# Kernel tuning notes

Hardware: AMD Instinct MI355X
Metric: run time of the kernel (lower is better)

## Reference

```python
import jax, jax.numpy as jnp
import numpy as np

K = 256
ALPHA = 0.2   # bml_alpha
BETA = 0.3    # bml_beta
EPS = 1e-8    # torch CosineSimilarity eps
NEG_INF = -10000.0
WEIGHT_TEMP = 0.05


def _l2n(x):
    # cosine-normalize rows, matching nn.CosineSimilarity's eps clamp
    n = jnp.linalg.norm(x, axis=-1, keepdims=True)
    return x / jnp.maximum(n, EPS)


def setup_inputs() -> dict:
    key = jax.random.key(0)
    k1, k2, k3 = jax.random.split(key, 3)
    B, D = 8192, 768
    datapoints = jax.random.normal(k1, (B, D), dtype=jnp.float32)
    centroid = jax.random.normal(k2, (K, D), dtype=jnp.float32)
    batch_cos_sim = jax.random.normal(k3, (B, B), dtype=jnp.float32)
    return {"datapoints": datapoints, "centroid": centroid, "batch_cos_sim": batch_cos_sim}


def reference(datapoints, centroid, batch_cos_sim):
    B = datapoints.shape[0]
    datapoints = jax.lax.stop_gradient(datapoints)  # forward() does clone().detach()

    # intra_cos_sim = cos(datapoints, centroid) / temp (temp=1)  -> [B, K]
    intra_cos_sim = _l2n(datapoints) @ _l2n(centroid).T

    # cluster assignment + intra-class adjacency
    dp_index = jnp.argmax(intra_cos_sim, axis=-1)                 # [B]
    onehot = jax.nn.one_hot(dp_index, K, dtype=jnp.float32)       # [B, K]
    dp_cluster = onehot @ onehot.T                                # [B, B]
    eye = jnp.eye(B, dtype=bool)
    dp_cluster = jnp.where(eye, 0.0, dp_cluster)                  # fill_diagonal_(0)

    # gather assigned centroid per datapoint
    dp_centroid = centroid[dp_index]                              # [B, D]

    # hard negative: 2nd-closest centroid (top-2 on cosine sim), detached
    _, top2_idx = jax.lax.top_k(intra_cos_sim, 2)                 # [B, 2]
    hard_negative = jax.lax.stop_gradient(centroid[top2_idx[:, 1]])  # [B, D]

    # false-negative BML loss on the in-batch cosine matrix
    pos = jnp.diagonal(batch_cos_sim)[:, None]                    # [B, 1]
    delta = (batch_cos_sim - pos) * dp_cluster                    # [B, B]
    fn_loss = (jax.nn.relu(delta + ALPHA) + jax.nn.relu(-delta - BETA)).mean()

    # softmax-weighted negatives (diag masked to -10000), detached
    masked = jnp.where(eye, NEG_INF, batch_cos_sim)
    weights = jax.lax.stop_gradient(jax.nn.softmax(masked, axis=-1) / WEIGHT_TEMP)

    return intra_cos_sim, dp_cluster, dp_centroid, hard_negative, fn_loss, weights
```

## Files before the change

kernel.cpp:

```cpp
#include <hip/hip_runtime.h>
#include <math.h>

#define B_N 8192
#define K_N 256
#define D_N 768

static constexpr float ALPHA_C = 0.2f;
static constexpr float BETA_C  = 0.3f;
static constexpr float EPS_C   = 1e-8f;
static constexpr float NEG_INF_C = -10000.0f;
static constexpr float INV_WTEMP = 20.0f;

__global__ __launch_bounds__(256) void k_centroid_prep(
        const float* __restrict__ centroid, float* __restrict__ cnt) {
    int c = blockIdx.x, t = threadIdx.x;
    const float* p = centroid + c * D_N;
    float v0 = p[t], v1 = p[t + 256], v2 = p[t + 512];
    float s = v0 * v0 + v1 * v1 + v2 * v2;
    #pragma unroll
    for (int o = 32; o >= 1; o >>= 1) s += __shfl_xor(s, o);
    __shared__ float red[4];
    __shared__ float sinv;
    if ((t & 63) == 0) red[t >> 6] = s;
    __syncthreads();
    if (t == 0)
        sinv = 1.0f / fmaxf(sqrtf(red[0] + red[1] + red[2] + red[3]), EPS_C);
    __syncthreads();
    float inv = sinv;
    cnt[(t)       * K_N + c] = v0 * inv;
    cnt[(t + 256) * K_N + c] = v1 * inv;
    cnt[(t + 512) * K_N + c] = v2 * inv;
}

__global__ __launch_bounds__(256) void k_rnorm(
        const float* __restrict__ dp, float* __restrict__ rnorm) {
    int i = blockIdx.x, t = threadIdx.x;
    const float* p = dp + (size_t)i * D_N;
    float v0 = p[t], v1 = p[t + 256], v2 = p[t + 512];
    float s = v0 * v0 + v1 * v1 + v2 * v2;
    #pragma unroll
    for (int o = 32; o >= 1; o >>= 1) s += __shfl_xor(s, o);
    __shared__ float red[4];
    if ((t & 63) == 0) red[t >> 6] = s;
    __syncthreads();
    if (t == 0) {
        float n = sqrtf(red[0] + red[1] + red[2] + red[3]);
        rnorm[i] = 1.0f / fmaxf(n, EPS_C);
    }
}

#define BM 32
#define KC 32
__global__ __launch_bounds__(256) void k_intra(
        const float* __restrict__ dp, const float* __restrict__ cnt,
        const float* __restrict__ rnorm, float* __restrict__ out) {
    __shared__ float ct[KC][K_N];
    __shared__ float dpt[KC][BM + 4];
    int t = threadIdx.x;
    int row0 = blockIdx.x * BM;
    int tx = t & 63, ty = t >> 6;
    int c0 = tx * 4;
    int r0 = ty * 8;

    float acc[8][4];
    #pragma unroll
    for (int r = 0; r < 8; ++r)
        #pragma unroll
        for (int c = 0; c < 4; ++c) acc[r][c] = 0.f;

    int sr = t >> 3, skq = t & 7;

    for (int kb = 0; kb < D_N; kb += KC) {
        __syncthreads();
        #pragma unroll
        for (int u = 0; u < 8; ++u) {
            int f4 = t + 256 * u;
            int k = f4 >> 6, c4 = (f4 & 63) << 2;
            *(float4*)&ct[k][c4] = *(const float4*)&cnt[(size_t)(kb + k) * K_N + c4];
        }
        {
            float4 v = *(const float4*)&dp[(size_t)(row0 + sr) * D_N + kb + skq * 4];
            dpt[skq * 4 + 0][sr] = v.x;
            dpt[skq * 4 + 1][sr] = v.y;
            dpt[skq * 4 + 2][sr] = v.z;
            dpt[skq * 4 + 3][sr] = v.w;
        }
        __syncthreads();
        #pragma unroll
        for (int k = 0; k < KC; ++k) {
            float4 b4 = *(float4*)&ct[k][c0];
            float4 a0 = *(float4*)&dpt[k][r0];
            float4 a1 = *(float4*)&dpt[k][r0 + 4];
            float a[8] = {a0.x, a0.y, a0.z, a0.w, a1.x, a1.y, a1.z, a1.w};
            float b[4] = {b4.x, b4.y, b4.z, b4.w};
            #pragma unroll
            for (int r = 0; r < 8; ++r)
                #pragma unroll
                for (int c = 0; c < 4; ++c)
                    acc[r][c] += a[r] * b[c];
        }
    }

    #pragma unroll
    for (int r = 0; r < 8; ++r) {
        float rn = rnorm[row0 + r0 + r];
        float4 o;
        o.x = acc[r][0] * rn; o.y = acc[r][1] * rn;
        o.z = acc[r][2] * rn; o.w = acc[r][3] * rn;
        *(float4*)&out[(size_t)(row0 + r0 + r) * K_N + c0] = o;
    }
}

__device__ __forceinline__ bool top_better(float v, int iv, float w, int iw) {
    return (v > w) || ((v == w) && (iv < iw));
}

__global__ __launch_bounds__(64) void k_top2(
        const float* __restrict__ intra, const float* __restrict__ centroid,
        unsigned char* __restrict__ cid,
        float* __restrict__ dp_centroid, float* __restrict__ hard_negative) {
    int i = blockIdx.x;
    int l = threadIdx.x;
    float m1 = -1e30f, m2 = -1e30f;
    int i1 = K_N, i2 = K_N;
    #pragma unroll
    for (int u = 0; u < 4; ++u) {
        int c = l + 64 * u;
        float v = intra[(size_t)i * K_N + c];
        if (v > m1) { m2 = m1; i2 = i1; m1 = v; i1 = c; }
        else if (v > m2) { m2 = v; i2 = c; }
    }
    #pragma unroll
    for (int o = 32; o >= 1; o >>= 1) {
        float om1 = __shfl_xor(m1, o);
        int   oi1 = __shfl_xor(i1, o);
        float om2 = __shfl_xor(m2, o);
        int   oi2 = __shfl_xor(i2, o);
        if (top_better(om1, oi1, m1, i1)) {
            if (top_better(m1, i1, om2, oi2)) { m2 = m1; i2 = i1; }
            else                              { m2 = om2; i2 = oi2; }
            m1 = om1; i1 = oi1;
        } else if (top_better(om1, oi1, m2, i2)) {
            m2 = om1; i2 = oi1;
        }
    }
    if (l == 0) cid[i] = (unsigned char)i1;

    const float4* s1 = (const float4*)(centroid + (size_t)i1 * D_N);
    const float4* s2 = (const float4*)(centroid + (size_t)i2 * D_N);
    float4* d1 = (float4*)(dp_centroid   + (size_t)i * D_N);
    float4* d2 = (float4*)(hard_negative + (size_t)i * D_N);
    #pragma unroll
    for (int u = 0; u < 3; ++u) {
        d1[l + 64 * u] = s1[l + 64 * u];
        d2[l + 64 * u] = s2[l + 64 * u];
    }
}

__global__ __launch_bounds__(256) void k_row(
        const float* __restrict__ bcs, const unsigned char* __restrict__ cid_g,
        float* __restrict__ dp_cluster, float* __restrict__ weights,
        double* __restrict__ acc) {
    int i = blockIdx.x;
    int t = threadIdx.x;
    __shared__ float4 row4[B_N / 4];
    __shared__ uint4  cid4[B_N / 16];
    __shared__ float  red[4];
    float* row = (float*)row4;
    const unsigned char* cid = (const unsigned char*)cid4;

    #pragma unroll
    for (int u = 0; u < 2; ++u)
        cid4[t + 256 * u] = ((const uint4*)cid_g)[t + 256 * u];

    const float4* src = (const float4*)(bcs + (size_t)i * B_N);
    float mx = -3.0e38f;
    #pragma unroll
    for (int u = 0; u < 8; ++u) {
        int f4 = t + 256 * u;
        float4 v = src[f4];
        row4[f4] = v;
        int j0 = f4 * 4;
        float a = (j0     == i) ? NEG_INF_C : v.x;
        float b = (j0 + 1 == i) ? NEG_INF_C : v.y;
        float c = (j0 + 2 == i) ? NEG_INF_C : v.z;
        float d = (j0 + 3 == i) ? NEG_INF_C : v.w;
        mx = fmaxf(mx, fmaxf(fmaxf(a, b), fmaxf(c, d)));
    }
    __syncthreads();
    #pragma unroll
    for (int o = 32; o >= 1; o >>= 1) mx = fmaxf(mx, __shfl_xor(mx, o));
    if ((t & 63) == 0) red[t >> 6] = mx;
    __syncthreads();
    mx = fmaxf(fmaxf(red[0], red[1]), fmaxf(red[2], red[3]));

    float pos = row[i];
    unsigned char myc = cid[i];
    __syncthreads();

    float fn = 0.f, se = 0.f;
    float* dcrow = dp_cluster + (size_t)i * B_N;
    #pragma unroll
    for (int r = 0; r < 8; ++r) {
        int f4 = t + 256 * r;
        int j0 = f4 * 4;
        float4 v = row4[f4];
        float4 e, dc;
        {
            bool same = (cid[j0] == myc) & (j0 != i);
            float delta = same ? (v.x - pos) : 0.f;
            fn += fmaxf(delta + ALPHA_C, 0.f) + fmaxf(-delta - BETA_C, 0.f);
            dc.x = same ? 1.0f : 0.f;
            e.x = __expf(((j0 == i) ? NEG_INF_C : v.x) - mx);
        }
        {
            bool same = (cid[j0 + 1] == myc) & (j0 + 1 != i);
            float delta = same ? (v.y - pos) : 0.f;
            fn += fmaxf(delta + ALPHA_C, 0.f) + fmaxf(-delta - BETA_C, 0.f);
            dc.y = same ? 1.0f : 0.f;
            e.y = __expf(((j0 + 1 == i) ? NEG_INF_C : v.y) - mx);
        }
        {
            bool same = (cid[j0 + 2] == myc) & (j0 + 2 != i);
            float delta = same ? (v.z - pos) : 0.f;
            fn += fmaxf(delta + ALPHA_C, 0.f) + fmaxf(-delta - BETA_C, 0.f);
            dc.z = same ? 1.0f : 0.f;
            e.z = __expf(((j0 + 2 == i) ? NEG_INF_C : v.z) - mx);
        }
        {
            bool same = (cid[j0 + 3] == myc) & (j0 + 3 != i);
            float delta = same ? (v.w - pos) : 0.f;
            fn += fmaxf(delta + ALPHA_C, 0.f) + fmaxf(-delta - BETA_C, 0.f);
            dc.w = same ? 1.0f : 0.f;
            e.w = __expf(((j0 + 3 == i) ? NEG_INF_C : v.w) - mx);
        }
        se += e.x + e.y + e.z + e.w;
        row4[f4] = e;
        ((float4*)dcrow)[f4] = dc;
    }

    #pragma unroll
    for (int o = 32; o >= 1; o >>= 1) se += __shfl_xor(se, o);
    if ((t & 63) == 0) red[t >> 6] = se;
    __syncthreads();
    se = red[0] + red[1] + red[2] + red[3];
    float inv = INV_WTEMP / se;

    float* wrow = weights + (size_t)i * B_N;
    #pragma unroll
    for (int r = 0; r < 32; ++r) {
        int j = t + 256 * r;
        wrow[j] = row[j] * inv;
    }

    #pragma unroll
    for (int o = 32; o >= 1; o >>= 1) fn += __shfl_xor(fn, o);
    __syncthreads();
    if ((t & 63) == 0) red[t >> 6] = fn;
    __syncthreads();
    if (t == 0) atomicAdd(acc, (double)(red[0] + red[1] + red[2] + red[3]));
}

__global__ void k_final(const double* __restrict__ acc, float* __restrict__ out) {
    out[0] = (float)(acc[0] / ((double)B_N * (double)B_N));
}

extern "C" void kernel_launch(void* const* d_in, const int* in_sizes, int n_in,
                              void* d_out, int out_size, void* d_ws, size_t ws_size,
                              hipStream_t stream) {
    const float* dp       = (const float*)d_in[0];
    const float* centroid = (const float*)d_in[1];
    const float* bcs      = (const float*)d_in[2];
    float* out = (float*)d_out;

    float* intra       = out;
    float* dp_cluster  = out + 2097152;
    float* dp_centroid = out + 69206016;
    float* hard_neg    = out + 75497472;
    float* fn_out      = out + 81788928;
    float* weights     = out + 81788929;

    char* ws = (char*)d_ws;
    double*        acc   = (double*)ws;
    float*         cnt   = (float*)(ws + 256);
    float*         rnorm = (float*)(ws + 256 + 786432);
    unsigned char* cid   = (unsigned char*)(ws + 256 + 786432 + 32768);

    hipMemsetAsync(acc, 0, sizeof(double), stream);
    k_centroid_prep<<<K_N, 256, 0, stream>>>(centroid, cnt);
    k_rnorm<<<B_N, 256, 0, stream>>>(dp, rnorm);
    k_intra<<<B_N / BM, 256, 0, stream>>>(dp, cnt, rnorm, intra);
    k_top2<<<B_N, 64, 0, stream>>>(intra, centroid, cid, dp_centroid, hard_neg);
    k_row<<<B_N, 256, 0, stream>>>(bcs, cid, dp_cluster, weights, acc);
    k_final<<<1, 1, 0, stream>>>(acc, fn_out);
}
```

Before: 244.1 us.

## Fuse row norms and top-2 gather into GEMM kernel, keep rows in registers

Computes the datapoint row norms inside the intra-similarity GEMM from the already-loaded tiles, and performs the top-2 selection and centroid gathers in the GEMM epilogue. This removes the separate rnorm and top2 kernels and a re-read of the intra matrix. The row kernel keeps the bcs row in registers instead of LDS and reads cluster ids as packed words. A last-block counter computes the final mean, replacing the final kernel. The risk is that the serialized epilogue loop and the scalar weight stores may limit bandwidth.

```diff
diff --git a/kernel.cpp b/kernel.cpp
--- a/kernel.cpp
+++ b/kernel.cpp
@@ -4,6 +4,8 @@
 #define B_N 8192
 #define K_N 256
 #define D_N 768
+#define BM 32
+#define KC 32
 
 static constexpr float ALPHA_C = 0.2f;
 static constexpr float BETA_C  = 0.3f;
@@ -32,43 +34,32 @@
     cnt[(t + 512) * K_N + c] = v2 * inv;
 }
 
-__global__ __launch_bounds__(256) void k_rnorm(
-        const float* __restrict__ dp, float* __restrict__ rnorm) {
-    int i = blockIdx.x, t = threadIdx.x;
-    const float* p = dp + (size_t)i * D_N;
-    float v0 = p[t], v1 = p[t + 256], v2 = p[t + 512];
-    float s = v0 * v0 + v1 * v1 + v2 * v2;
-    #pragma unroll
-    for (int o = 32; o >= 1; o >>= 1) s += __shfl_xor(s, o);
-    __shared__ float red[4];
-    if ((t & 63) == 0) red[t >> 6] = s;
-    __syncthreads();
-    if (t == 0) {
-        float n = sqrtf(red[0] + red[1] + red[2] + red[3]);
-        rnorm[i] = 1.0f / fmaxf(n, EPS_C);
-    }
-}
-
-#define BM 32
-#define KC 32
+__device__ __forceinline__ bool top_better(float v, int iv, float w, int iw) {
+    return (v > w) || ((v == w) && (iv < iw));
+}
+
 __global__ __launch_bounds__(256) void k_intra(
         const float* __restrict__ dp, const float* __restrict__ cnt,
-        const float* __restrict__ rnorm, float* __restrict__ out) {
+        const float* __restrict__ centroid,
+        float* __restrict__ out_intra, unsigned char* __restrict__ cid_g,
+        float* __restrict__ dp_centroid, float* __restrict__ hard_negative) {
     __shared__ float ct[KC][K_N];
     __shared__ float dpt[KC][BM + 4];
+    __shared__ float sqp[BM][8];
+    __shared__ float rn[BM];
     int t = threadIdx.x;
     int row0 = blockIdx.x * BM;
     int tx = t & 63, ty = t >> 6;
     int c0 = tx * 4;
     int r0 = ty * 8;
+    int sr = t >> 3, skq = t & 7;
 
     float acc[8][4];
     #pragma unroll
     for (int r = 0; r < 8; ++r)
         #pragma unroll
         for (int c = 0; c < 4; ++c) acc[r][c] = 0.f;
-
-    int sr = t >> 3, skq = t & 7;
+    float ss = 0.f;
 
     for (int kb = 0; kb < D_N; kb += KC) {
         __syncthreads();
@@ -80,6 +71,7 @@
         }
         {
             float4 v = *(const float4*)&dp[(size_t)(row0 + sr) * D_N + kb + skq * 4];
+            ss += v.x * v.x + v.y * v.y + v.z * v.z + v.w * v.w;
             dpt[skq * 4 + 0][sr] = v.x;
             dpt[skq * 4 + 1][sr] = v.y;
             dpt[skq * 4 + 2][sr] = v.z;
@@ -101,91 +93,95 @@
         }
     }
 
-    #pragma unroll
+    sqp[sr][skq] = ss;
+    __syncthreads();
+    if (t < BM) {
+        float s = 0.f;
+        #pragma unroll
+        for (int j = 0; j < 8; ++j) s += sqp[t][j];
+        rn[t] = 1.0f / fmaxf(sqrtf(s), EPS_C);
+    }
+    __syncthreads();
+
+    #pragma unroll 1
     for (int r = 0; r < 8; ++r) {
-        float rn = rnorm[row0 + r0 + r];
+        int row = row0 + r0 + r;
+        float rv = rn[r0 + r];
         float4 o;
-        o.x = acc[r][0] * rn; o.y = acc[r][1] * rn;
-        o.z = acc[r][2] * rn; o.w = acc[r][3] * rn;
-        *(float4*)&out[(size_t)(row0 + r0 + r) * K_N + c0] = o;
-    }
-}
-
-__device__ __forceinline__ bool top_better(float v, int iv, float w, int iw) {
-    return (v > w) || ((v == w) && (iv < iw));
-}
-
-__global__ __launch_bounds__(64) void k_top2(
-        const float* __restrict__ intra, const float* __restrict__ centroid,
-        unsigned char* __restrict__ cid,
-        float* __restrict__ dp_centroid, float* __restrict__ hard_negative) {
-    int i = blockIdx.x;
-    int l = threadIdx.x;
-    float m1 = -1e30f, m2 = -1e30f;
-    int i1 = K_N, i2 = K_N;
-    #pragma unroll
-    for (int u = 0; u < 4; ++u) {
-        int c = l + 64 * u;
-        float v = intra[(size_t)i * K_N + c];
-        if (v > m1) { m2 = m1; i2 = i1; m1 = v; i1 = c; }
-        else if (v > m2) { m2 = v; i2 = c; }
-    }
-    #pragma unroll
-    for (int o = 32; o >= 1; o >>= 1) {
-        float om1 = __shfl_xor(m1, o);
-        int   oi1 = __shfl_xor(i1, o);
-        float om2 = __shfl_xor(m2, o);
-        int   oi2 = __shfl_xor(i2, o);
-        if (top_better(om1, oi1, m1, i1)) {
-            if (top_better(m1, i1, om2, oi2)) { m2 = m1; i2 = i1; }
-            else                              { m2 = om2; i2 = oi2; }
-            m1 = om1; i1 = oi1;
-        } else if (top_better(om1, oi1, m2, i2)) {
-            m2 = om1; i2 = oi1;
-        }
-    }
-    if (l == 0) cid[i] = (unsigned char)i1;
-
-    const float4* s1 = (const float4*)(centroid + (size_t)i1 * D_N);
-    const float4* s2 = (const float4*)(centroid + (size_t)i2 * D_N);
-    float4* d1 = (float4*)(dp_centroid   + (size_t)i * D_N);
-    float4* d2 = (float4*)(hard_negative + (size_t)i * D_N);
-    #pragma unroll
-    for (int u = 0; u < 3; ++u) {
-        d1[l + 64 * u] = s1[l + 64 * u];
-        d2[l + 64 * u] = s2[l + 64 * u];
+        o.x = acc[r][0] * rv; o.y = acc[r][1] * rv;
+        o.z = acc[r][2] * rv; o.w = acc[r][3] * rv;
+        *(float4*)&out_intra[(size_t)row * K_N + c0] = o;
+
+        float m1 = o.x, m2 = -1e30f;
+        int i1 = c0, i2 = K_N;
+        { float v = o.y; int id = c0 + 1;
+          if (v > m1) { m2 = m1; i2 = i1; m1 = v; i1 = id; } else if (v > m2) { m2 = v; i2 = id; } }
+        { float v = o.z; int id = c0 + 2;
+          if (v > m1) { m2 = m1; i2 = i1; m1 = v; i1 = id; } else if (v > m2) { m2 = v; i2 = id; } }
+        { float v = o.w; int id = c0 + 3;
+          if (v > m1) { m2 = m1; i2 = i1; m1 = v; i1 = id; } else if (v > m2) { m2 = v; i2 = id; } }
+        #pragma unroll
+        for (int off = 32; off >= 1; off >>= 1) {
+            float om1 = __shfl_xor(m1, off);
+            int   oi1 = __shfl_xor(i1, off);
+            float om2 = __shfl_xor(m2, off);
+            int   oi2 = __shfl_xor(i2, off);
+            if (top_better(om1, oi1, m1, i1)) {
+                if (top_better(m1, i1, om2, oi2)) { m2 = m1; i2 = i1; }
+                else                              { m2 = om2; i2 = oi2; }
+                m1 = om1; i1 = oi1;
+            } else if (top_better(om1, oi1, m2, i2)) {
+                m2 = om1; i2 = oi1;
+            }
+        }
+        if (tx == 0) cid_g[row] = (unsigned char)i1;
+
+        const float4* s1 = (const float4*)(centroid + (size_t)i1 * D_N);
+        const float4* s2 = (const float4*)(centroid + (size_t)i2 * D_N);
+        float4* d1 = (float4*)(dp_centroid   + (size_t)row * D_N);
+        float4* d2 = (float4*)(hard_negative + (size_t)row * D_N);
+        #pragma unroll
+        for (int u = 0; u < 3; ++u) {
+            d1[tx + 64 * u] = s1[tx + 64 * u];
+            d2[tx + 64 * u] = s2[tx + 64 * u];
+        }
     }
 }
 
 __global__ __launch_bounds__(256) void k_row(
         const float* __restrict__ bcs, const unsigned char* __restrict__ cid_g,
         float* __restrict__ dp_cluster, float* __restrict__ weights,
-        double* __restrict__ acc) {
+        double* __restrict__ accd, unsigned int* __restrict__ counter,
+        float* __restrict__ fn_out) {
     int i = blockIdx.x;
     int t = threadIdx.x;
-    __shared__ float4 row4[B_N / 4];
-    __shared__ uint4  cid4[B_N / 16];
-    __shared__ float  red[4];
-    float* row = (float*)row4;
-    const unsigned char* cid = (const unsigned char*)cid4;
+    __shared__ uint4 cid4[B_N / 16];
+    __shared__ float red[4];
+    __shared__ float posb;
+    const unsigned* cidw = (const unsigned*)cid4;
 
     #pragma unroll
     for (int u = 0; u < 2; ++u)
         cid4[t + 256 * u] = ((const uint4*)cid_g)[t + 256 * u];
 
     const float4* src = (const float4*)(bcs + (size_t)i * B_N);
+    float4 v[8];
     float mx = -3.0e38f;
     #pragma unroll
     for (int u = 0; u < 8; ++u) {
         int f4 = t + 256 * u;
-        float4 v = src[f4];
-        row4[f4] = v;
+        v[u] = src[f4];
         int j0 = f4 * 4;
-        float a = (j0     == i) ? NEG_INF_C : v.x;
-        float b = (j0 + 1 == i) ? NEG_INF_C : v.y;
-        float c = (j0 + 2 == i) ? NEG_INF_C : v.z;
-        float d = (j0 + 3 == i) ? NEG_INF_C : v.w;
+        float a = (j0     == i) ? NEG_INF_C : v[u].x;
+        float b = (j0 + 1 == i) ? NEG_INF_C : v[u].y;
+        float c = (j0 + 2 == i) ? NEG_INF_C : v[u].z;
+        float d = (j0 + 3 == i) ? NEG_INF_C : v[u].w;
         mx = fmaxf(mx, fmaxf(fmaxf(a, b), fmaxf(c, d)));
+        if (j0 <= i && i < j0 + 4) {
+            int q = i - j0;
+            float pe = (q == 0) ? v[u].x : ((q == 1) ? v[u].y : ((q == 2) ? v[u].z : v[u].w));
+            posb = pe;
+        }
     }
     __syncthreads();
     #pragma unroll
@@ -193,49 +189,48 @@
     if ((t & 63) == 0) red[t >> 6] = mx;
     __syncthreads();
     mx = fmaxf(fmaxf(red[0], red[1]), fmaxf(red[2], red[3]));
-
-    float pos = row[i];
-    unsigned char myc = cid[i];
+    float pos = posb;
+    unsigned myc = (cidw[i >> 2] >> ((i & 3) * 8)) & 255u;
     __syncthreads();
 
     float fn = 0.f, se = 0.f;
     float* dcrow = dp_cluster + (size_t)i * B_N;
     #pragma unroll
-    for (int r = 0; r < 8; ++r) {
-        int f4 = t + 256 * r;
+    for (int u = 0; u < 8; ++u) {
+        int f4 = t + 256 * u;
         int j0 = f4 * 4;
-        float4 v = row4[f4];
-        float4 e, dc;
-        {
-            bool same = (cid[j0] == myc) & (j0 != i);
-            float delta = same ? (v.x - pos) : 0.f;
+        unsigned cw = cidw[f4];
+        float4 w = v[u], e, dc;
+        {
+            bool same = ((cw & 255u) == myc) & (j0 != i);
+            float delta = same ? (w.x - pos) : 0.f;
             fn += fmaxf(delta + ALPHA_C, 0.f) + fmaxf(-delta - BETA_C, 0.f);
             dc.x = same ? 1.0f : 0.f;
-            e.x = __expf(((j0 == i) ? NEG_INF_C : v.x) - mx);
-        }
-        {
-            bool same = (cid[j0 + 1] == myc) & (j0 + 1 != i);
-            float delta = same ? (v.y - pos) : 0.f;
+            e.x = __expf(((j0 == i) ? NEG_INF_C : w.x) - mx);
+        }
+        {
+            bool same = (((cw >> 8) & 255u) == myc) & (j0 + 1 != i);
+            float delta = same ? (w.y - pos) : 0.f;
             fn += fmaxf(delta + ALPHA_C, 0.f) + fmaxf(-delta - BETA_C, 0.f);
             dc.y = same ? 1.0f : 0.f;
-            e.y = __expf(((j0 + 1 == i) ? NEG_INF_C : v.y) - mx);
-        }
-        {
-            bool same = (cid[j0 + 2] == myc) & (j0 + 2 != i);
-            float delta = same ? (v.z - pos) : 0.f;
+            e.y = __expf(((j0 + 1 == i) ? NEG_INF_C : w.y) - mx);
+        }
+        {
+            bool same = (((cw >> 16) & 255u) == myc) & (j0 + 2 != i);
+            float delta = same ? (w.z - pos) : 0.f;
             fn += fmaxf(delta + ALPHA_C, 0.f) + fmaxf(-delta - BETA_C, 0.f);
             dc.z = same ? 1.0f : 0.f;
-            e.z = __expf(((j0 + 2 == i) ? NEG_INF_C : v.z) - mx);
-        }
-        {
-            bool same = (cid[j0 + 3] == myc) & (j0 + 3 != i);
-            float delta = same ? (v.w - pos) : 0.f;
+            e.z = __expf(((j0 + 2 == i) ? NEG_INF_C : w.z) - mx);
+        }
+        {
+            bool same = (((cw >> 24) & 255u) == myc) & (j0 + 3 != i);
+            float delta = same ? (w.w - pos) : 0.f;
             fn += fmaxf(delta + ALPHA_C, 0.f) + fmaxf(-delta - BETA_C, 0.f);
             dc.w = same ? 1.0f : 0.f;
-            e.w = __expf(((j0 + 3 == i) ? NEG_INF_C : v.w) - mx);
+            e.w = __expf(((j0 + 3 == i) ? NEG_INF_C : w.w) - mx);
         }
         se += e.x + e.y + e.z + e.w;
-        row4[f4] = e;
+        v[u] = e;
         ((float4*)dcrow)[f4] = dc;
     }
 
@@ -248,9 +243,12 @@
 
     float* wrow = weights + (size_t)i * B_N;
     #pragma unroll
-    for (int r = 0; r < 32; ++r) {
-        int j = t + 256 * r;
-        wrow[j] = row[j] * inv;
+    for (int u = 0; u < 8; ++u) {
+        int j0 = (t + 256 * u) * 4;
+        wrow[j0]     = v[u].x * inv;
+        wrow[j0 + 1] = v[u].y * inv;
+        wrow[j0 + 2] = v[u].z * inv;
+        wrow[j0 + 3] = v[u].w * inv;
     }
 
     #pragma unroll
@@ -258,11 +256,15 @@
     __syncthreads();
     if ((t & 63) == 0) red[t >> 6] = fn;
     __syncthreads();
-    if (t == 0) atomicAdd(acc, (double)(red[0] + red[1] + red[2] + red[3]));
-}
-
-__global__ void k_final(const double* __restrict__ acc, float* __restrict__ out) {
-    out[0] = (float)(acc[0] / ((double)B_N * (double)B_N));
+    if (t == 0) {
+        atomicAdd(accd, (double)(red[0] + red[1] + red[2] + red[3]));
+        __threadfence();
+        unsigned done = atomicAdd(counter, 1u);
+        if (done == (unsigned)(gridDim.x - 1)) {
+            double total = atomicAdd(accd, 0.0);
+            fn_out[0] = (float)(total / ((double)B_N * (double)B_N));
+        }
+    }
 }
 
 extern "C" void kernel_launch(void* const* d_in, const int* in_sizes, int n_in,
@@ -281,16 +283,14 @@
     float* weights     = out + 81788929;
 
     char* ws = (char*)d_ws;
-    double*        acc   = (double*)ws;
-    float*         cnt   = (float*)(ws + 256);
-    float*         rnorm = (float*)(ws + 256 + 786432);
-    unsigned char* cid   = (unsigned char*)(ws + 256 + 786432 + 32768);
-
-    hipMemsetAsync(acc, 0, sizeof(double), stream);
+    double*        acc     = (double*)ws;
+    unsigned int*  counter = (unsigned int*)(ws + 8);
+    float*         cnt     = (float*)(ws + 256);
+    unsigned char* cid     = (unsigned char*)(ws + 256 + 786432);
+
+    hipMemsetAsync(ws, 0, 16, stream);
     k_centroid_prep<<<K_N, 256, 0, stream>>>(centroid, cnt);
-    k_rnorm<<<B_N, 256, 0, stream>>>(dp, rnorm);
-    k_intra<<<B_N / BM, 256, 0, stream>>>(dp, cnt, rnorm, intra);
-    k_top2<<<B_N, 64, 0, stream>>>(intra, centroid, cid, dp_centroid, hard_neg);
-    k_row<<<B_N, 256, 0, stream>>>(bcs, cid, dp_cluster, weights, acc);
-    k_final<<<1, 1, 0, stream>>>(acc, fn_out);
-}
+    k_intra<<<B_N / BM, 256, 0, stream>>>(dp, cnt, centroid, intra, cid,
+                                          dp_centroid, hard_neg);
+    k_row<<<B_N, 256, 0, stream>>>(bcs, cid, dp_cluster, weights, acc, counter, fn_out);
+}
```

After: 722.4 us. +195.9%, slower.
